# Optimization experiments

Measured on AMD Instinct MI355X. Metric: run time of the kernel, lower is better.

The kernel has to match this reference:

```python
import jax, jax.numpy as jnp
import numpy as np


def setup_inputs() -> dict:
    key = jax.random.key(0)
    k1, k2, k3 = jax.random.split(key, 3)
    N = 524288
    T, C, R = 32, 7, 512
    texcoord = jax.random.uniform(k1, (N, 2), dtype=jnp.float32, minval=-1.0, maxval=1.0)
    mix_weights = jax.random.normal(k2, (N, T), dtype=jnp.float32)
    textures = jax.random.normal(k3, (T, C, R, R), dtype=jnp.float32)
    return {"texcoord": texcoord, "mix_weights": mix_weights, "textures": textures}


def _mixed_bilinear(texcoord, mix_weights, textures):
    # Faithful to F.grid_sample(mode='bilinear', padding_mode='zeros', align_corners=False)
    # followed by the mix-weight reduction over the texture dim, fused per corner.
    T, C, H, W = textures.shape
    in_shape = texcoord.shape
    tc = texcoord.reshape(-1, 2)           # [N, 2], (x, y) with x indexing W
    mw = mix_weights.reshape(-1, T)        # [N, T]

    x, y = tc[:, 0], tc[:, 1]
    # unnormalize (align_corners=False): pixel = ((coord + 1) * size - 1) / 2
    ix = ((x + 1.0) * W - 1.0) * 0.5
    iy = ((y + 1.0) * H - 1.0) * 0.5
    x0 = jnp.floor(ix)
    y0 = jnp.floor(iy)
    x1 = x0 + 1.0
    y1 = y0 + 1.0

    out = jnp.zeros((tc.shape[0], C), dtype=textures.dtype)
    corners = [
        (x0, y0, (x1 - ix) * (y1 - iy)),
        (x1, y0, (ix - x0) * (y1 - iy)),
        (x0, y1, (x1 - ix) * (iy - y0)),
        (x1, y1, (ix - x0) * (iy - y0)),
    ]
    for cx, cy, cw in corners:
        valid = (cx >= 0) & (cx <= W - 1) & (cy >= 0) & (cy <= H - 1)  # zeros padding
        xi = jnp.clip(cx, 0, W - 1).astype(jnp.int32)
        yi = jnp.clip(cy, 0, H - 1).astype(jnp.int32)
        g = textures[:, :, yi, xi]                      # [T, C, N] gather
        w = jnp.where(valid, cw, 0.0)                    # [N]
        out = out + jnp.einsum('n,nt,tcn->nc', w, mw, g)
    return out.reshape(in_shape[:-1] + (C,))


def reference(texcoord, mix_weights, textures):
    return _mixed_bilinear(texcoord, mix_weights, textures)
```

## Files before the change

kernel.cpp:

```cpp
#include <hip/hip_runtime.h>
#include <hip/hip_fp16.h>


#define RR 512
#define TT 32
#define CC 7
#define CAP 256
#define NBK 4096
#define CHUNKS_PER_C 324
#define CSTRIDE 325

typedef float fx2 __attribute__((ext_vector_type(2)));
typedef float fx4 __attribute__((ext_vector_type(4)));
typedef _Float16 h2 __attribute__((ext_vector_type(2)));

__global__ __launch_bounds__(256) void zero_cursor(int* __restrict__ cursor) {
    cursor[blockIdx.x * 256 + threadIdx.x] = 0;
}

__global__ __launch_bounds__(256) void transpose_tex(const float* __restrict__ src,
                                                     uint4* __restrict__ dst) {
    __shared__ float tile[32 * 68];
    int b  = blockIdx.x;
    int xb = (b & 7) << 6;
    int y  = (b >> 3) & 511;
    int c  = b >> 12;
    int tid = threadIdx.x;

    const fx4* s4 = (const fx4*)src;
#pragma unroll
    for (int p = 0; p < 2; ++p) {
        int q  = p * 256 + tid;
        int t  = q >> 4;
        int xv = q & 15;
        fx4 v = s4[(size_t)(((t * 7 + c) * 512 + y) * 512 + xb) / 4 + xv];
        *(fx4*)&tile[t * 68 + 4 * xv] = v;
    }
    __syncthreads();

    int x  = tid >> 2;
    int t8 = tid & 3;
    union { uint4 u; __half2 h[4]; } U;
#pragma unroll
    for (int j2 = 0; j2 < 4; ++j2) {
        float lo = tile[(t8 * 8 + 2 * j2) * 68 + x];
        float hi = tile[(t8 * 8 + 2 * j2 + 1) * 68 + x];
        U.h[j2] = __floats2half2_rn(lo, hi);
    }
    dst[(size_t)((c * 512 + y) * 512 + xb + x) * 4 + t8] = U.u;
}

__global__ __launch_bounds__(256) void scatter_direct(const fx2* __restrict__ tc2,
                                                      fx4* __restrict__ recs,
                                                      int* __restrict__ cursor, int N) {
    int n = blockIdx.x * 256 + threadIdx.x;
    if (n >= N) return;
    fx2 xy = tc2[n];
    float ix = ((xy.x + 1.0f) * 512.0f - 1.0f) * 0.5f;
    float iy = ((xy.y + 1.0f) * 512.0f - 1.0f) * 0.5f;
    int xi0 = (int)fminf(fmaxf(floorf(ix), 0.0f), 511.0f);
    int yi0 = (int)fminf(fmaxf(floorf(iy), 0.0f), 511.0f);
    int b = ((yi0 >> 3) << 6) | (xi0 >> 3);
    int slot = atomicAdd(&cursor[b << 4], 1);
    if (slot < CAP) {
        fx4 rec = {xy.x, xy.y, __int_as_float(n), 0.0f};
        recs[(size_t)b * CAP + slot] = rec;
    }
}

__device__ __forceinline__ float dot_pos(const uint4* __restrict__ T, int idx,
                                         const h2* __restrict__ mh) {
    float d = 0.0f;
#pragma unroll
    for (int q = 0; q < 4; ++q) {
        union { uint4 u; h2 h[4]; } U;
        U.u = T[idx + q];
#pragma unroll
        for (int j = 0; j < 4; ++j) {
#if __has_builtin(__builtin_amdgcn_fdot2)
            d = __builtin_amdgcn_fdot2(U.h[j], mh[q * 4 + j], d, false);
#else
            d += (float)U.h[j].x * (float)mh[q * 4 + j].x
               + (float)U.h[j].y * (float)mh[q * 4 + j].y;
#endif
        }
    }
    return d;
}

__global__ __launch_bounds__(256) void mix_tile(const fx4* __restrict__ recs,
                                                const int* __restrict__ cnts,
                                                const fx4* __restrict__ mw4,
                                                const uint4* __restrict__ t16,
                                                float* __restrict__ out) {
    __shared__ uint4 TILE[7 * CSTRIDE];
    int k  = blockIdx.x;
    int tx = k & 63, ty = k >> 6;
    int X0 = tx << 3, Y0 = ty << 3;
    int tid = threadIdx.x;

    for (int q = tid; q < 7 * CHUNKS_PER_C; q += 256) {
        int c  = q / CHUNKS_PER_C;
        int r  = q - c * CHUNKS_PER_C;
        int yy = r / 36;
        int rr = r - yy * 36;
        int gx = X0 + (rr >> 2); if (gx > 511) gx = 511;
        int gy = Y0 + yy;        if (gy > 511) gy = 511;
        TILE[q + c] = t16[(size_t)((((c << 9) + gy) << 9) | gx) * 4 + (rr & 3)];
    }
    __syncthreads();

    int cnt = cnts[k << 4]; if (cnt > CAP) cnt = CAP;
    int sub = tid & 7;
    int c   = (sub == 7) ? 0 : sub;
    int cbase = c * CSTRIDE;
    size_t rbase = (size_t)k * CAP;

    int s = tid >> 3;
    if (s >= cnt) return;

    fx4 rec = recs[rbase + s];
    int n = __float_as_int(rec.z);
    fx4 m[8];
#pragma unroll
    for (int j = 0; j < 8; ++j) m[j] = mw4[(size_t)n * 8 + j];

    while (true) {
        int s2 = s + 32;
        bool live2 = s2 < cnt;
        fx4 rec2 = rec;
        if (live2) rec2 = recs[rbase + s2];

        float ix = ((rec.x + 1.0f) * 512.0f - 1.0f) * 0.5f;
        float iy = ((rec.y + 1.0f) * 512.0f - 1.0f) * 0.5f;
        float x0f = floorf(ix), y0f = floorf(iy);
        float fxw = ix - x0f, fyw = iy - y0f;
        float gxw = 1.0f - fxw, gyw = 1.0f - fyw;
        float w00 = gxw * gyw, w10 = fxw * gyw, w01 = gxw * fyw, w11 = fxw * fyw;
        bool vx0 = (x0f >= 0.0f), vx1 = (x0f <= 510.0f);
        bool vy0 = (y0f >= 0.0f), vy1 = (y0f <= 510.0f);
        if (!(vx0 && vy0)) w00 = 0.0f;
        if (!(vx1 && vy0)) w10 = 0.0f;
        if (!(vx0 && vy1)) w01 = 0.0f;
        if (!(vx1 && vy1)) w11 = 0.0f;
        int xi0 = (int)fminf(fmaxf(x0f, 0.0f), 511.0f);
        int xi1 = (int)fminf(fmaxf(x0f + 1.0f, 0.0f), 511.0f);
        int yi0 = (int)fminf(fmaxf(y0f, 0.0f), 511.0f);
        int yi1 = (int)fminf(fmaxf(y0f + 1.0f, 0.0f), 511.0f);
        int xl0 = xi0 - X0, xl1 = xi1 - X0;
        int yl0 = yi0 - Y0, yl1 = yi1 - Y0;

        h2 mh[16];
#pragma unroll
        for (int j = 0; j < 8; ++j) {
            mh[2 * j]     = h2{(_Float16)m[j].x, (_Float16)m[j].y};
            mh[2 * j + 1] = h2{(_Float16)m[j].z, (_Float16)m[j].w};
        }

        int p00 = cbase + ((yl0 * 9 + xl0) << 2);
        int p10 = cbase + ((yl0 * 9 + xl1) << 2);
        int p01 = cbase + ((yl1 * 9 + xl0) << 2);
        int p11 = cbase + ((yl1 * 9 + xl1) << 2);
        float d = w00 * dot_pos(TILE, p00, mh)
                + w10 * dot_pos(TILE, p10, mh)
                + w01 * dot_pos(TILE, p01, mh)
                + w11 * dot_pos(TILE, p11, mh);

        int nst = n;

        int n2 = 0;
        if (live2) {
            n2 = __float_as_int(rec2.z);
#pragma unroll
            for (int j = 0; j < 8; ++j) m[j] = mw4[(size_t)n2 * 8 + j];
        }

        if (sub < 7) __builtin_nontemporal_store(d, &out[(size_t)nst * 7 + c]);

        if (!live2) break;
        rec = rec2; n = n2; s = s2;
    }
}

__global__ __launch_bounds__(256) void mix_naive(const float* __restrict__ tc,
                                                 const float* __restrict__ mw,
                                                 const float* __restrict__ tex,
                                                 float* __restrict__ out, int N) {
    int n = blockIdx.x * 256 + threadIdx.x;
    if (n >= N) return;
    float x = tc[2 * n], y = tc[2 * n + 1];
    float ix = ((x + 1.0f) * 512.0f - 1.0f) * 0.5f;
    float iy = ((y + 1.0f) * 512.0f - 1.0f) * 0.5f;
    float x0f = floorf(ix), y0f = floorf(iy);
    float fx = ix - x0f, fy = iy - y0f;
    float gx = 1.0f - fx, gy = 1.0f - fy;
    float wgt[4] = {gx * gy, fx * gy, gx * fy, fx * fy};
    bool vx0 = (x0f >= 0.0f), vx1 = (x0f <= 510.0f);
    bool vy0 = (y0f >= 0.0f), vy1 = (y0f <= 510.0f);
    if (!(vx0 && vy0)) wgt[0] = 0.0f;
    if (!(vx1 && vy0)) wgt[1] = 0.0f;
    if (!(vx0 && vy1)) wgt[2] = 0.0f;
    if (!(vx1 && vy1)) wgt[3] = 0.0f;
    int xi0 = (int)fminf(fmaxf(x0f, 0.0f), 511.0f);
    int xi1 = (int)fminf(fmaxf(x0f + 1.0f, 0.0f), 511.0f);
    int yi0 = (int)fminf(fmaxf(y0f, 0.0f), 511.0f);
    int yi1 = (int)fminf(fmaxf(y0f + 1.0f, 0.0f), 511.0f);
    int xs[4] = {xi0, xi1, xi0, xi1};
    int ys[4] = {yi0, yi0, yi1, yi1};

    float acc[7] = {0.f, 0.f, 0.f, 0.f, 0.f, 0.f, 0.f};
#pragma unroll
    for (int kk = 0; kk < 4; ++kk) {
        float wk = wgt[kk];
        int base = ys[kk] * 512 + xs[kk];
        for (int t = 0; t < 32; ++t) {
            float m = wk * mw[(size_t)n * 32 + t];
#pragma unroll
            for (int cc = 0; cc < 7; ++cc)
                acc[cc] = fmaf(m, tex[(t * 7 + cc) * 262144 + base], acc[cc]);
        }
    }
#pragma unroll
    for (int cc = 0; cc < 7; ++cc) out[(size_t)n * 7 + cc] = acc[cc];
}

extern "C" void kernel_launch(void* const* d_in, const int* in_sizes, int n_in,
                              void* d_out, int out_size, void* d_ws, size_t ws_size,
                              hipStream_t stream) {
    const float* tc  = (const float*)d_in[0];
    const float* mw  = (const float*)d_in[1];
    const float* tex = (const float*)d_in[2];
    float* out = (float*)d_out;
    int N = in_sizes[0] / 2;

    const size_t TEXB = (size_t)CC * RR * RR * TT * sizeof(__half);
    const size_t RECB = (size_t)NBK * CAP * sizeof(fx4);
    const size_t CURB = (size_t)NBK * 16 * sizeof(int);
    const size_t need = TEXB + RECB + CURB;

    if (ws_size >= need) {
        char* ws = (char*)d_ws;
        uint4* wst  = (uint4*)ws;
        fx4*   recs = (fx4*)(ws + TEXB);
        int*   cur  = (int*)(ws + TEXB + RECB);

        zero_cursor<<<NBK * 16 / 256, 256, 0, stream>>>(cur);
        scatter_direct<<<(N + 255) / 256, 256, 0, stream>>>((const fx2*)tc, recs, cur, N);
        transpose_tex<<<7 * 512 * 8, 256, 0, stream>>>(tex, wst);
        mix_tile<<<NBK, 256, 0, stream>>>((const fx4*)recs, (const int*)cur,
                                          (const fx4*)mw, (const uint4*)wst, out);
    } else {
        mix_naive<<<(N + 255) / 256, 256, 0, stream>>>(tc, mw, tex, out, N);
    }
}
```

Measured before the change: 176.6 us.

## Store only point indices in bucket records and prefetch inputs one step ahead

Bucket records shrink from a 16-byte (x, y, n) vector to a single int index, cutting write and read traffic in the scatter and mix kernels. The mix kernel now fetches texcoords by index and prefetches the next point's coordinates and fp16-converted mix weights (and the index two steps ahead), loading mix weights with nontemporal hints. The cost is an extra dependent gather of texcoords and higher register pressure from the doubled mix-weight buffers.

Result: slower. 182.9 us (+3.5%).

```diff
diff --git a/kernel.cpp b/kernel.cpp
--- a/kernel.cpp
+++ b/kernel.cpp
@@ -51,7 +51,7 @@
 }
 
 __global__ __launch_bounds__(256) void scatter_direct(const fx2* __restrict__ tc2,
-                                                      fx4* __restrict__ recs,
+                                                      int* __restrict__ recs,
                                                       int* __restrict__ cursor, int N) {
     int n = blockIdx.x * 256 + threadIdx.x;
     if (n >= N) return;
@@ -62,10 +62,7 @@
     int yi0 = (int)fminf(fmaxf(floorf(iy), 0.0f), 511.0f);
     int b = ((yi0 >> 3) << 6) | (xi0 >> 3);
     int slot = atomicAdd(&cursor[b << 4], 1);
-    if (slot < CAP) {
-        fx4 rec = {xy.x, xy.y, __int_as_float(n), 0.0f};
-        recs[(size_t)b * CAP + slot] = rec;
-    }
+    if (slot < CAP) recs[b * CAP + slot] = n;
 }
 
 __device__ __forceinline__ float dot_pos(const uint4* __restrict__ T, int idx,
@@ -88,8 +85,19 @@
     return d;
 }
 
-__global__ __launch_bounds__(256) void mix_tile(const fx4* __restrict__ recs,
+__device__ __forceinline__ void load_mh(const fx4* __restrict__ mw4, int n,
+                                        h2* __restrict__ mh) {
+#pragma unroll
+    for (int j = 0; j < 8; ++j) {
+        fx4 m = __builtin_nontemporal_load(&mw4[(size_t)n * 8 + j]);
+        mh[2 * j]     = h2{(_Float16)m.x, (_Float16)m.y};
+        mh[2 * j + 1] = h2{(_Float16)m.z, (_Float16)m.w};
+    }
+}
+
+__global__ __launch_bounds__(256) void mix_tile(const int* __restrict__ recs,
                                                 const int* __restrict__ cnts,
+                                                const fx2* __restrict__ tc2,
                                                 const fx4* __restrict__ mw4,
                                                 const uint4* __restrict__ t16,
                                                 float* __restrict__ out) {
@@ -114,25 +122,32 @@
     int sub = tid & 7;
     int c   = (sub == 7) ? 0 : sub;
     int cbase = c * CSTRIDE;
-    size_t rbase = (size_t)k * CAP;
+    int rbase = k * CAP;
 
     int s = tid >> 3;
     if (s >= cnt) return;
 
-    fx4 rec = recs[rbase + s];
-    int n = __float_as_int(rec.z);
-    fx4 m[8];
-#pragma unroll
-    for (int j = 0; j < 8; ++j) m[j] = mw4[(size_t)n * 8 + j];
+    int n_cur = recs[rbase + s];
+    fx2 xy_cur = tc2[n_cur];
+    h2 mh_cur[16];
+    load_mh(mw4, n_cur, mh_cur);
+    int s1 = s + 32;
+    int n_nxt = (s1 < cnt) ? recs[rbase + s1] : 0;
 
     while (true) {
-        int s2 = s + 32;
-        bool live2 = s2 < cnt;
-        fx4 rec2 = rec;
-        if (live2) rec2 = recs[rbase + s2];
-
-        float ix = ((rec.x + 1.0f) * 512.0f - 1.0f) * 0.5f;
-        float iy = ((rec.y + 1.0f) * 512.0f - 1.0f) * 0.5f;
+        bool live1 = (s1 < cnt);
+        int  s2    = s1 + 32;
+        int  n_nn  = (s2 < cnt) ? recs[rbase + s2] : 0;
+
+        fx2 xy_nxt;
+        h2  mh_nxt[16];
+        if (live1) {
+            xy_nxt = tc2[n_nxt];
+            load_mh(mw4, n_nxt, mh_nxt);
+        }
+
+        float ix = ((xy_cur.x + 1.0f) * 512.0f - 1.0f) * 0.5f;
+        float iy = ((xy_cur.y + 1.0f) * 512.0f - 1.0f) * 0.5f;
         float x0f = floorf(ix), y0f = floorf(iy);
         float fxw = ix - x0f, fyw = iy - y0f;
         float gxw = 1.0f - fxw, gyw = 1.0f - fyw;
@@ -150,35 +165,23 @@
         int xl0 = xi0 - X0, xl1 = xi1 - X0;
         int yl0 = yi0 - Y0, yl1 = yi1 - Y0;
 
-        h2 mh[16];
-#pragma unroll
-        for (int j = 0; j < 8; ++j) {
-            mh[2 * j]     = h2{(_Float16)m[j].x, (_Float16)m[j].y};
-            mh[2 * j + 1] = h2{(_Float16)m[j].z, (_Float16)m[j].w};
-        }
-
         int p00 = cbase + ((yl0 * 9 + xl0) << 2);
         int p10 = cbase + ((yl0 * 9 + xl1) << 2);
         int p01 = cbase + ((yl1 * 9 + xl0) << 2);
         int p11 = cbase + ((yl1 * 9 + xl1) << 2);
-        float d = w00 * dot_pos(TILE, p00, mh)
-                + w10 * dot_pos(TILE, p10, mh)
-                + w01 * dot_pos(TILE, p01, mh)
-                + w11 * dot_pos(TILE, p11, mh);
-
-        int nst = n;
-
-        int n2 = 0;
-        if (live2) {
-            n2 = __float_as_int(rec2.z);
-#pragma unroll
-            for (int j = 0; j < 8; ++j) m[j] = mw4[(size_t)n2 * 8 + j];
-        }
-
-        if (sub < 7) __builtin_nontemporal_store(d, &out[(size_t)nst * 7 + c]);
-
-        if (!live2) break;
-        rec = rec2; n = n2; s = s2;
+        float d = w00 * dot_pos(TILE, p00, mh_cur)
+                + w10 * dot_pos(TILE, p10, mh_cur)
+                + w01 * dot_pos(TILE, p01, mh_cur)
+                + w11 * dot_pos(TILE, p11, mh_cur);
+
+        if (sub < 7) __builtin_nontemporal_store(d, &out[(size_t)n_cur * 7 + c]);
+
+        if (!live1) break;
+        n_cur = n_nxt; xy_cur = xy_nxt;
+#pragma unroll
+        for (int j = 0; j < 16; ++j) mh_cur[j] = mh_nxt[j];
+        n_nxt = n_nn;
+        s1 = s2;
     }
 }
 
@@ -234,21 +237,22 @@
     int N = in_sizes[0] / 2;
 
     const size_t TEXB = (size_t)CC * RR * RR * TT * sizeof(__half);
-    const size_t RECB = (size_t)NBK * CAP * sizeof(fx4);
+    const size_t RECB = (size_t)NBK * CAP * sizeof(int);
     const size_t CURB = (size_t)NBK * 16 * sizeof(int);
     const size_t need = TEXB + RECB + CURB;
 
     if (ws_size >= need) {
         char* ws = (char*)d_ws;
         uint4* wst  = (uint4*)ws;
-        fx4*   recs = (fx4*)(ws + TEXB);
+        int*   recs = (int*)(ws + TEXB);
         int*   cur  = (int*)(ws + TEXB + RECB);
 
         zero_cursor<<<NBK * 16 / 256, 256, 0, stream>>>(cur);
         scatter_direct<<<(N + 255) / 256, 256, 0, stream>>>((const fx2*)tc, recs, cur, N);
         transpose_tex<<<7 * 512 * 8, 256, 0, stream>>>(tex, wst);
-        mix_tile<<<NBK, 256, 0, stream>>>((const fx4*)recs, (const int*)cur,
-                                          (const fx4*)mw, (const uint4*)wst, out);
+        mix_tile<<<NBK, 256, 0, stream>>>((const int*)recs, (const int*)cur,
+                                          (const fx2*)tc, (const fx4*)mw,
+                                          (const uint4*)wst, out);
     } else {
         mix_naive<<<(N + 255) / 256, 256, 0, stream>>>(tc, mw, tex, out, N);
     }
```

## Fuse texture fp16 transpose into mix_tile tile loading

Applied to the files above, without the earlier changes.

Removes the separate transpose kernel that converted the whole fp32 texture array to a t-interleaved fp16 copy. mix_tile now gathers its 9x9 neighbourhood directly from the original fp32 layout, converting to half2 while filling shared memory. This saves one full write and reread of the texture copy and a launch. In exchange, the tile loads become many strided scalar loads (one per texture index) with poor coalescing, and overlapping tile halos are reread in fp32.

Result: slower. 277.7 us (+57.2%).

```diff
diff --git a/kernel.cpp b/kernel.cpp
--- a/kernel.cpp
+++ b/kernel.cpp
@@ -7,8 +7,8 @@
 #define CC 7
 #define CAP 256
 #define NBK 4096
-#define CHUNKS_PER_C 324
 #define CSTRIDE 325
+#define TSTRIDE 1835008
 
 typedef float fx2 __attribute__((ext_vector_type(2)));
 typedef float fx4 __attribute__((ext_vector_type(4)));
@@ -16,38 +16,6 @@
 
 __global__ __launch_bounds__(256) void zero_cursor(int* __restrict__ cursor) {
     cursor[blockIdx.x * 256 + threadIdx.x] = 0;
-}
-
-__global__ __launch_bounds__(256) void transpose_tex(const float* __restrict__ src,
-                                                     uint4* __restrict__ dst) {
-    __shared__ float tile[32 * 68];
-    int b  = blockIdx.x;
-    int xb = (b & 7) << 6;
-    int y  = (b >> 3) & 511;
-    int c  = b >> 12;
-    int tid = threadIdx.x;
-
-    const fx4* s4 = (const fx4*)src;
-#pragma unroll
-    for (int p = 0; p < 2; ++p) {
-        int q  = p * 256 + tid;
-        int t  = q >> 4;
-        int xv = q & 15;
-        fx4 v = s4[(size_t)(((t * 7 + c) * 512 + y) * 512 + xb) / 4 + xv];
-        *(fx4*)&tile[t * 68 + 4 * xv] = v;
-    }
-    __syncthreads();
-
-    int x  = tid >> 2;
-    int t8 = tid & 3;
-    union { uint4 u; __half2 h[4]; } U;
-#pragma unroll
-    for (int j2 = 0; j2 < 4; ++j2) {
-        float lo = tile[(t8 * 8 + 2 * j2) * 68 + x];
-        float hi = tile[(t8 * 8 + 2 * j2 + 1) * 68 + x];
-        U.h[j2] = __floats2half2_rn(lo, hi);
-    }
-    dst[(size_t)((c * 512 + y) * 512 + xb + x) * 4 + t8] = U.u;
 }
 
 __global__ __launch_bounds__(256) void scatter_direct(const fx2* __restrict__ tc2,
@@ -91,7 +59,7 @@
 __global__ __launch_bounds__(256) void mix_tile(const fx4* __restrict__ recs,
                                                 const int* __restrict__ cnts,
                                                 const fx4* __restrict__ mw4,
-                                                const uint4* __restrict__ t16,
+                                                const float* __restrict__ src,
                                                 float* __restrict__ out) {
     __shared__ uint4 TILE[7 * CSTRIDE];
     int k  = blockIdx.x;
@@ -99,14 +67,23 @@
     int X0 = tx << 3, Y0 = ty << 3;
     int tid = threadIdx.x;
 
-    for (int q = tid; q < 7 * CHUNKS_PER_C; q += 256) {
-        int c  = q / CHUNKS_PER_C;
-        int r  = q - c * CHUNKS_PER_C;
-        int yy = r / 36;
-        int rr = r - yy * 36;
-        int gx = X0 + (rr >> 2); if (gx > 511) gx = 511;
-        int gy = Y0 + yy;        if (gy > 511) gy = 511;
-        TILE[q + c] = t16[(size_t)((((c << 9) + gy) << 9) | gx) * 4 + (rr & 3)];
+    for (int i = tid; i < 7 * 81 * 4; i += 256) {
+        int c = i / 324;
+        int r = i - c * 324;
+        int v = r >> 2;
+        int q = r & 3;
+        int yy = v / 9, xx = v - yy * 9;
+        int gx = X0 + xx; if (gx > 511) gx = 511;
+        int gy = Y0 + yy; if (gy > 511) gy = 511;
+        const float* rb = src + ((size_t)(8 * q * 7 + c) * 512 + gy) * 512 + gx;
+        union { uint4 u; __half2 h[4]; } U;
+#pragma unroll
+        for (int j = 0; j < 4; ++j) {
+            float lo = rb[(size_t)(2 * j) * TSTRIDE];
+            float hi = rb[(size_t)(2 * j + 1) * TSTRIDE];
+            U.h[j] = __floats2half2_rn(lo, hi);
+        }
+        TILE[c * CSTRIDE + v * 4 + q] = U.u;
     }
     __syncthreads();
 
@@ -233,22 +210,19 @@
     float* out = (float*)d_out;
     int N = in_sizes[0] / 2;
 
-    const size_t TEXB = (size_t)CC * RR * RR * TT * sizeof(__half);
     const size_t RECB = (size_t)NBK * CAP * sizeof(fx4);
     const size_t CURB = (size_t)NBK * 16 * sizeof(int);
-    const size_t need = TEXB + RECB + CURB;
+    const size_t need = RECB + CURB;
 
     if (ws_size >= need) {
         char* ws = (char*)d_ws;
-        uint4* wst  = (uint4*)ws;
-        fx4*   recs = (fx4*)(ws + TEXB);
-        int*   cur  = (int*)(ws + TEXB + RECB);
+        fx4* recs = (fx4*)ws;
+        int* cur  = (int*)(ws + RECB);
 
         zero_cursor<<<NBK * 16 / 256, 256, 0, stream>>>(cur);
         scatter_direct<<<(N + 255) / 256, 256, 0, stream>>>((const fx2*)tc, recs, cur, N);
-        transpose_tex<<<7 * 512 * 8, 256, 0, stream>>>(tex, wst);
         mix_tile<<<NBK, 256, 0, stream>>>((const fx4*)recs, (const int*)cur,
-                                          (const fx4*)mw, (const uint4*)wst, out);
+                                          (const fx4*)mw, tex, out);
     } else {
         mix_naive<<<(N + 255) / 256, 256, 0, stream>>>(tc, mw, tex, out, N);
     }
```
